# Optimization experiments

Measured on AMD Instinct MI355X. Metric: run time of the kernel, lower is better.

## Reference

```python
import jax, jax.numpy as jnp
import numpy as np

N = 20000        # nodes per type (ant, user)
E = 400000       # edges per relation
F_IN = 128       # args.user_num -> input feature dim
H = 10           # attention heads
D1, D2 = 16, 32  # per-head out channels of HGT layers 1 and 2
H1, H2 = H * D1, H * D2  # 160, 320


def _segment_softmax(logit, dst, n):
    m = jax.ops.segment_max(logit, dst, num_segments=n)
    e = jnp.exp(logit - m[dst])
    s = jax.ops.segment_sum(e, dst, num_segments=n)
    return e / (s[dst] + 1e-16)


def _hgt_layer(x_a, x_u, ei_au, ea_au, ei_ua, ea_ua,
               kw, kb, qw, qb, vw, vb, arel, mrel, prel, ew, eb, alw, alb, D):
    # per-node-type K/Q/V projections, reshaped to [N, H, D]
    def proj(x, w, b, i):
        return (x @ w[i] + b[i]).reshape(x.shape[0], H, D)
    k_a, q_a, v_a = proj(x_a, kw, kb, 0), proj(x_a, qw, qb, 0), proj(x_a, vw, vb, 0)
    k_u, q_u, v_u = proj(x_u, kw, kb, 1), proj(x_u, qw, qb, 1), proj(x_u, vw, vb, 1)
    scale = 1.0 / jnp.sqrt(jnp.float32(D))

    def relation(k_s, v_s, q_d, ei, ea, r, n_dst):
        # apply per-relation matrices at node granularity (cheaper than per-edge)
        kr = jnp.einsum('nhd,hde->nhe', k_s, arel[r])
        vr = jnp.einsum('nhd,hde->nhe', v_s, mrel[r])
        src, dst = ei[0], ei[1]
        # [E, H] attention logits: HGT dot-product * relation prior + edge-attr term
        logit = (q_d[dst] * kr[src]).sum(-1) * scale * prel[r] + ea @ ew[r] + eb[r]
        a = _segment_softmax(logit, dst, n_dst)
        msg = vr[src] * a[..., None]                        # [E, H, D]
        out = jax.ops.segment_sum(msg, dst, num_segments=n_dst)
        return out.reshape(n_dst, H * D)

    agg_u = relation(k_a, v_a, q_u, ei_au, ea_au, 0, x_u.shape[0])  # ant -> user
    agg_a = relation(k_u, v_u, q_a, ei_ua, ea_ua, 1, x_a.shape[0])  # user -> ant
    out_a = jax.nn.gelu(agg_a) @ alw[0] + alb[0]
    out_u = jax.nn.gelu(agg_u) @ alw[1] + alb[1]
    return out_a, out_u


def _bn(x, g, b):
    mu = x.mean(0)
    var = x.var(0)
    return (x - mu) / jnp.sqrt(var + 1e-5) * g + b


def _forward(x_ant, x_user, ea_au, ea_ua,
             l1_kw, l1_kb, l1_qw, l1_qb, l1_vw, l1_vb, l1_arel, l1_mrel, l1_prel, l1_ew, l1_eb, l1_alw, l1_alb,
             l2_kw, l2_kb, l2_qw, l2_qb, l2_vw, l2_vb, l2_arel, l2_mrel, l2_prel, l2_ew, l2_eb, l2_alw, l2_alb,
             lin1_w, lin1_b, bn_g, bn_b, lin2_wa, lin2_ba, lin2_wu, lin2_bu,
             ei_au, ei_ua):
    a, u = _hgt_layer(x_ant, x_user, ei_au, ea_au, ei_ua, ea_ua,
                      l1_kw, l1_kb, l1_qw, l1_qb, l1_vw, l1_vb,
                      l1_arel, l1_mrel, l1_prel, l1_ew, l1_eb, l1_alw, l1_alb, D1)
    a, u = jax.nn.elu(a), jax.nn.elu(u)
    a, u = _hgt_layer(a, u, ei_au, ea_au, ei_ua, ea_ua,
                      l2_kw, l2_kb, l2_qw, l2_qb, l2_vw, l2_vb,
                      l2_arel, l2_mrel, l2_prel, l2_ew, l2_eb, l2_alw, l2_alb, D2)
    a, u = jax.nn.elu(a), jax.nn.elu(u)
    a = jax.nn.elu(a @ lin1_w[0] + lin1_b[0])
    u = jax.nn.elu(u @ lin1_w[1] + lin1_b[1])
    a = _bn(a, bn_g[0], bn_b[0])
    u = _bn(u, bn_g[1], bn_b[1])
    a = a @ lin2_wa + lin2_ba       # [N, user_num]   beamforming weights
    u = u @ lin2_wu + lin2_bu       # [N, user_num+1] assignment logits
    # MM_Dict_ACT: power-normalize ant outputs, softmax user assignments
    a = a / jnp.sqrt((a * a).sum(-1, keepdims=True) + 1e-12)
    u = jax.nn.softmax(u, axis=-1)
    return a, u


def setup_inputs() -> dict:
    key = jax.random.key(0)
    ks = iter(jax.random.split(key, 64))
    nk = lambda: next(ks)
    rn = lambda shape, s=0.05: jax.random.normal(nk(), shape, dtype=jnp.float32) * s
    inp = {}
    inp['x_ant'] = rn((N, F_IN), 1.0)
    inp['x_user'] = rn((N, F_IN), 1.0)
    inp['ea_au'] = jax.random.uniform(nk(), (E, 1), dtype=jnp.float32)
    inp['ea_ua'] = jax.random.uniform(nk(), (E, 1), dtype=jnp.float32)

    def hgt_params(p, fin, d):
        hd = H * d
        inp[p + 'kw'] = rn((2, fin, hd)); inp[p + 'kb'] = jnp.zeros((2, hd))
        inp[p + 'qw'] = rn((2, fin, hd)); inp[p + 'qb'] = jnp.zeros((2, hd))
        inp[p + 'vw'] = rn((2, fin, hd)); inp[p + 'vb'] = jnp.zeros((2, hd))
        inp[p + 'arel'] = rn((2, H, d, d), 0.2)
        inp[p + 'mrel'] = rn((2, H, d, d), 0.2)
        inp[p + 'prel'] = jnp.ones((2, H), dtype=jnp.float32)
        inp[p + 'ew'] = rn((2, 1, H)); inp[p + 'eb'] = jnp.zeros((2, H))
        inp[p + 'alw'] = rn((2, hd, hd)); inp[p + 'alb'] = jnp.zeros((2, hd))

    hgt_params('l1_', F_IN, D1)
    hgt_params('l2_', H1, D2)
    inp['lin1_w'] = rn((2, H2, 512)); inp['lin1_b'] = jnp.zeros((2, 512))
    inp['bn_g'] = jnp.ones((2, 512), dtype=jnp.float32)
    inp['bn_b'] = jnp.zeros((2, 512), dtype=jnp.float32)
    inp['lin2_wa'] = rn((512, F_IN)); inp['lin2_ba'] = jnp.zeros((F_IN,))
    inp['lin2_wu'] = rn((512, F_IN + 1)); inp['lin2_bu'] = jnp.zeros((F_IN + 1,))
    inp['ei_au'] = jax.random.randint(nk(), (2, E), 0, N)
    inp['ei_ua'] = jax.random.randint(nk(), (2, E), 0, N)
    return inp


def reference(x_ant, x_user, ea_au, ea_ua,
              l1_kw, l1_kb, l1_qw, l1_qb, l1_vw, l1_vb, l1_arel, l1_mrel, l1_prel, l1_ew, l1_eb, l1_alw, l1_alb,
              l2_kw, l2_kb, l2_qw, l2_qb, l2_vw, l2_vb, l2_arel, l2_mrel, l2_prel, l2_ew, l2_eb, l2_alw, l2_alb,
              lin1_w, lin1_b, bn_g, bn_b, lin2_wa, lin2_ba, lin2_wu, lin2_bu,
              ei_au, ei_ua):
    return _forward(x_ant, x_user, ea_au, ea_ua,
                    l1_kw, l1_kb, l1_qw, l1_qb, l1_vw, l1_vb, l1_arel, l1_mrel, l1_prel, l1_ew, l1_eb, l1_alw, l1_alb,
                    l2_kw, l2_kb, l2_qw, l2_qb, l2_vw, l2_vb, l2_arel, l2_mrel, l2_prel, l2_ew, l2_eb, l2_alw, l2_alb,
                    lin1_w, lin1_b, bn_g, bn_b, lin2_wa, lin2_ba, lin2_wu, lin2_bu,
                    ei_au, ei_ua)
```

## Files before the change

kernel.cpp:

```cpp
#include <hip/hip_runtime.h>
#include <hip/hip_bf16.h>
#include <math.h>

#define N_NODES 20000
#define N_EDGES 400000
#define NH 10

typedef __attribute__((ext_vector_type(8))) short short8v;
typedef __attribute__((ext_vector_type(4))) float f32x4;

__device__ __forceinline__ float gelu_f(float x) {
    float x3 = x * x * x;
    return 0.5f * x * (1.0f + tanhf(0.7978845608028654f * (x + 0.044715f * x3)));
}
__device__ __forceinline__ float elu_f(float x) {
    return x > 0.0f ? x : (expf(x) - 1.0f);
}
__device__ __forceinline__ float bf_lo(unsigned int w) {
    return __uint_as_float(w << 16);
}
__device__ __forceinline__ float bf_hi(unsigned int w) {
    return __uint_as_float(w & 0xffff0000u);
}
__device__ __forceinline__ unsigned short f2b(float x) {
    unsigned int u = __float_as_uint(x);
    return (unsigned short)((u + 0x7fffu + ((u >> 16) & 1u)) >> 16);
}

struct GemmPair {
    const __hip_bfloat16 *A0, *A1, *W0, *W1;
    const float *b0, *b1;
    void *C0, *C1;
    int N0, N1;
};
template<int ACT, typename OUT>
__global__ __launch_bounds__(256) void gemm2_kernel(GemmPair P, int M, int K)
{
    constexpr int PITCH = 40;
    __shared__ __align__(16) unsigned short As[128 * PITCH];
    __shared__ __align__(16) unsigned short Bs[128 * PITCH];
    const int z = blockIdx.z;
    const __hip_bfloat16* A  = z ? P.A1 : P.A0;
    const __hip_bfloat16* WT = z ? P.W1 : P.W0;
    const float* bias = z ? P.b1 : P.b0;
    OUT* C = (OUT*)(z ? P.C1 : P.C0);
    const int N = z ? P.N1 : P.N0;

    const int tid = threadIdx.x;
    const int m0 = blockIdx.y * 128, n0 = blockIdx.x * 128;
    if (n0 >= N) return;
    const int w = tid >> 6, l = tid & 63;
    const int wr = w >> 1, wc = w & 1;
    const int lr = l & 15, lk = l >> 4;

    const int srow = tid >> 1, sseg = (tid & 1) * 16;
    const bool ainb = (m0 + srow) < M;
    const bool binb = (n0 + srow) < N;
    const __hip_bfloat16* aptr = A + (size_t)(m0 + srow) * K + sseg;
    const __hip_bfloat16* bptr = WT + (size_t)(n0 + srow) * K + sseg;

    int4 ra0, ra1, rb0, rb1;
    auto ld = [&](int k0) {
        ra0 = ainb ? *reinterpret_cast<const int4*>(aptr + k0)     : make_int4(0, 0, 0, 0);
        ra1 = ainb ? *reinterpret_cast<const int4*>(aptr + k0 + 8) : make_int4(0, 0, 0, 0);
        rb0 = binb ? *reinterpret_cast<const int4*>(bptr + k0)     : make_int4(0, 0, 0, 0);
        rb1 = binb ? *reinterpret_cast<const int4*>(bptr + k0 + 8) : make_int4(0, 0, 0, 0);
    };

    f32x4 acc[4][4] = {};
    ld(0);
    for (int k0 = 0; k0 < K; k0 += 32) {
        *reinterpret_cast<int4*>(&As[srow * PITCH + sseg])     = ra0;
        *reinterpret_cast<int4*>(&As[srow * PITCH + sseg + 8]) = ra1;
        *reinterpret_cast<int4*>(&Bs[srow * PITCH + sseg])     = rb0;
        *reinterpret_cast<int4*>(&Bs[srow * PITCH + sseg + 8]) = rb1;
        __syncthreads();
        if (k0 + 32 < K) ld(k0 + 32);
        short8v a[4], b[4];
        #pragma unroll
        for (int mi = 0; mi < 4; ++mi)
            a[mi] = *reinterpret_cast<const short8v*>(
                &As[(wr * 64 + mi * 16 + lr) * PITCH + lk * 8]);
        #pragma unroll
        for (int ni = 0; ni < 4; ++ni)
            b[ni] = *reinterpret_cast<const short8v*>(
                &Bs[(wc * 64 + ni * 16 + lr) * PITCH + lk * 8]);
        #pragma unroll
        for (int mi = 0; mi < 4; ++mi)
            #pragma unroll
            for (int ni = 0; ni < 4; ++ni)
                acc[mi][ni] = __builtin_amdgcn_mfma_f32_16x16x32_bf16(
                    a[mi], b[ni], acc[mi][ni], 0, 0, 0);
        __syncthreads();
    }
    #pragma unroll
    for (int ni = 0; ni < 4; ++ni) {
        const int col = n0 + wc * 64 + ni * 16 + lr;
        if (col >= N) continue;
        const float bv = bias[col];
        #pragma unroll
        for (int mi = 0; mi < 4; ++mi) {
            const int rb = m0 + wr * 64 + mi * 16 + lk * 4;
            #pragma unroll
            for (int j = 0; j < 4; ++j) {
                const int m = rb + j;
                if (m >= M) continue;
                float v = acc[mi][ni][j] + bv;
                if (ACT == 1) v = elu_f(v);
                if constexpr (sizeof(OUT) == 2)
                    C[(size_t)m * N + col] = __float2bfloat16(v);
                else
                    C[(size_t)m * N + col] = v;
            }
        }
    }
}

__global__ void transpose2_kernel(const float* in0, const float* in1,
                                  __hip_bfloat16* out0, __hip_bfloat16* out1,
                                  int K0, int N0, int K1, int N1)
{
    __shared__ float tile[32][33];
    const int z = blockIdx.z;
    const float* in = z ? in1 : in0;
    __hip_bfloat16* out = z ? out1 : out0;
    const int K = z ? K1 : K0, N = z ? N1 : N0;
    const int nb = blockIdx.x * 32, kb = blockIdx.y * 32;
    if (nb >= N || kb >= K) return;
    const int tx = threadIdx.x & 31, ty = threadIdx.x >> 5;
    for (int j = ty; j < 32; j += 8) {
        int k = kb + j, n = nb + tx;
        tile[j][tx] = (k < K && n < N) ? in[(size_t)k * N + n] : 0.f;
    }
    __syncthreads();
    for (int j = ty; j < 32; j += 8) {
        int n = nb + j, k = kb + tx;
        if (n < N && k < K) out[(size_t)n * K + k] = __float2bfloat16(tile[tx][j]);
    }
}

__global__ void convert_in_kernel(const float* __restrict__ in0, const float* __restrict__ in1,
                                  __hip_bfloat16* __restrict__ out0,
                                  __hip_bfloat16* __restrict__ out1, int n4)
{
    int i = blockIdx.x * blockDim.x + threadIdx.x;
    if (i >= n4) return;
    const float* in = blockIdx.y ? in1 : in0;
    __hip_bfloat16* out = blockIdx.y ? out1 : out0;
    float4 v = reinterpret_cast<const float4*>(in)[i];
    ushort4 b;
    b.x = f2b(v.x); b.y = f2b(v.y); b.z = f2b(v.z); b.w = f2b(v.w);
    reinterpret_cast<ushort4*>(out)[i] = b;
}

__global__ void prep_qkv2_kernel(const float* __restrict__ qw, const float* __restrict__ qb,
                                 const float* __restrict__ kw, const float* __restrict__ kb,
                                 const float* __restrict__ vw, const float* __restrict__ vb,
                                 const float* __restrict__ arel, const float* __restrict__ mrel,
                                 __hip_bfloat16* __restrict__ WT0, float* __restrict__ B0,
                                 __hip_bfloat16* __restrict__ WT1, float* __restrict__ B1,
                                 int fin, int D, int HD)
{
    const int type = blockIdx.y;
    const size_t woff = (size_t)type * fin * HD;
    const size_t roff = (size_t)type * NH * D * D;
    __hip_bfloat16* WT = type ? WT1 : WT0;
    float* BIAS = type ? B1 : B0;
    const int F1 = fin + 1;
    int tid = blockIdx.x * blockDim.x + threadIdx.x;
    if (tid >= 3 * HD * F1) return;
    const int f = tid % F1;
    const int col3 = tid / F1;
    const int sec = col3 / HD;
    const int col = col3 - sec * HD;
    float val;
    if (sec == 0) {
        val = (f < fin) ? qw[woff + (size_t)f * HD + col] : qb[type * HD + col];
    } else {
        const float* W = (sec == 1) ? kw : vw;
        const float* B = (sec == 1) ? kb : vb;
        const float* R = ((sec == 1) ? arel : mrel) + roff;
        const int h = col / D, e = col - h * D;
        const float* src = (f < fin) ? W + woff + (size_t)f * HD + h * D
                                     : B + type * HD + h * D;
        const float* r = R + (size_t)h * D * D + e;
        float acc = 0.f;
        for (int d = 0; d < D; ++d) acc = fmaf(src[d], r[(size_t)d * D], acc);
        val = acc;
    }
    if (f < fin) WT[(size_t)col3 * fin + f] = __float2bfloat16(val);
    else         BIAS[col3] = val;
}

template<int D>
__global__ __launch_bounds__(256) void edge_fused_kernel(
    const __hip_bfloat16* __restrict__ Ta, const __hip_bfloat16* __restrict__ Tu,
    const int* __restrict__ rp0, const int* __restrict__ src0, const float* __restrict__ eav0,
    const int* __restrict__ rp1, const int* __restrict__ src1, const float* __restrict__ eav1,
    const float* __restrict__ prel, const float* __restrict__ ew,
    const float* __restrict__ eb,
    __hip_bfloat16* __restrict__ outA, __hip_bfloat16* __restrict__ outU,
    float scale)
{
    constexpr int HD = NH * D;
    constexpr int S = 3 * HD;
    constexpr int C = 64;
    constexpr int POS = HD / 8;
    constexpr int G = (POS * 8 <= 256) ? 8 : 4;
    __shared__ float q_s[HD];
    __shared__ float ls[C][NH];
    __shared__ int   srcs[C];
    __shared__ float eas[C];
    __shared__ float prel_s[NH], ew_s[NH], eb_s[NH];

    const int b = blockIdx.x;
    const int rel = b & 1, dst = b >> 1;
    const int t = threadIdx.x;
    const __hip_bfloat16* Tkv = rel ? Tu : Ta;
    const __hip_bfloat16* Tq  = rel ? Ta : Tu;
    const int* rp    = rel ? rp1 : rp0;
    const int* srcA  = rel ? src1 : src0;
    const float* eav = rel ? eav1 : eav0;
    __hip_bfloat16* out = rel ? outA : outU;

    const int s0 = rp[dst], deg = rp[dst + 1] - s0;

    {
        const unsigned int* qrow = (const unsigned int*)(Tq + (size_t)dst * S);
        for (int i = t; i < HD / 2; i += 256) {
            unsigned int wd = qrow[i];
            q_s[2 * i]     = bf_lo(wd);
            q_s[2 * i + 1] = bf_hi(wd);
        }
    }
    if (t < NH) { prel_s[t] = prel[rel * NH + t]; ew_s[t] = ew[rel * NH + t];
                  eb_s[t] = eb[rel * NH + t]; }
    const int apos = t / G, ag = t % G;
    const int ah = (apos * 8) / D;
    float a8[8] = {};
    float ssum = 0.f;
    __syncthreads();

    for (int base = 0; base < deg; base += C) {
        const int cl = min(C, deg - base);
        if (t < cl) {
            srcs[t] = srcA[s0 + base + t];
            eas[t]  = eav[s0 + base + t];
        }
        __syncthreads();
        for (int item = t; item < cl * NH; item += 256) {
            const int p = item / NH, h = item - p * NH;
            const uint4* kr = (const uint4*)(Tkv + (size_t)srcs[p] * S + HD + h * D);
            const float* qh = q_s + h * D;
            float d0 = 0.f;
            #pragma unroll
            for (int c4 = 0; c4 < D / 8; ++c4) {
                const uint4 wd = kr[c4];
                const float* qq = qh + c4 * 8;
                d0 = fmaf(qq[0], bf_lo(wd.x), d0); d0 = fmaf(qq[1], bf_hi(wd.x), d0);
                d0 = fmaf(qq[2], bf_lo(wd.y), d0); d0 = fmaf(qq[3], bf_hi(wd.y), d0);
                d0 = fmaf(qq[4], bf_lo(wd.z), d0); d0 = fmaf(qq[5], bf_hi(wd.z), d0);
                d0 = fmaf(qq[6], bf_lo(wd.w), d0); d0 = fmaf(qq[7], bf_hi(wd.w), d0);
            }
            ls[p][h] = expf(d0 * scale * prel_s[h] + eas[p] * ew_s[h] + eb_s[h]);
        }
        __syncthreads();
        if (apos < POS) {
            for (int p = ag; p < cl; p += G) {
                const uint4* vr = (const uint4*)(Tkv + (size_t)srcs[p] * S + 2 * HD);
                const uint4 wd = vr[apos];
                const float wgt = ls[p][ah];
                ssum += wgt;
                a8[0] = fmaf(wgt, bf_lo(wd.x), a8[0]); a8[1] = fmaf(wgt, bf_hi(wd.x), a8[1]);
                a8[2] = fmaf(wgt, bf_lo(wd.y), a8[2]); a8[3] = fmaf(wgt, bf_hi(wd.y), a8[3]);
                a8[4] = fmaf(wgt, bf_lo(wd.z), a8[4]); a8[5] = fmaf(wgt, bf_hi(wd.z), a8[5]);
                a8[6] = fmaf(wgt, bf_lo(wd.w), a8[6]); a8[7] = fmaf(wgt, bf_hi(wd.w), a8[7]);
            }
        }
        __syncthreads();
    }
    if (apos < POS) {
        #pragma unroll
        for (int off = G / 2; off; off >>= 1) {
            #pragma unroll
            for (int j = 0; j < 8; ++j) a8[j] += __shfl_xor(a8[j], off);
            ssum += __shfl_xor(ssum, off);
        }
        if (ag == 0) {
            const float inv = 1.f / (ssum + 1e-16f);
            uint4 o;
            o.x = (unsigned int)f2b(gelu_f(a8[0] * inv)) |
                  ((unsigned int)f2b(gelu_f(a8[1] * inv)) << 16);
            o.y = (unsigned int)f2b(gelu_f(a8[2] * inv)) |
                  ((unsigned int)f2b(gelu_f(a8[3] * inv)) << 16);
            o.z = (unsigned int)f2b(gelu_f(a8[4] * inv)) |
                  ((unsigned int)f2b(gelu_f(a8[5] * inv)) << 16);
            o.w = (unsigned int)f2b(gelu_f(a8[6] * inv)) |
                  ((unsigned int)f2b(gelu_f(a8[7] * inv)) << 16);
            ((uint4*)(out + (size_t)dst * HD))[apos] = o;
        }
    }
}

__global__ void count2_kernel(const int* __restrict__ ei0, const int* __restrict__ ei1,
                              int* __restrict__ cnt0, int* __restrict__ cnt1)
{
    int e = blockIdx.x * blockDim.x + threadIdx.x;
    if (e >= N_EDGES) return;
    if (blockIdx.y == 0) atomicAdd(&cnt0[ei0[N_EDGES + e]], 1);
    else                 atomicAdd(&cnt1[ei1[N_EDGES + e]], 1);
}

__global__ void scatter2_kernel(const int* __restrict__ ei0, const float* __restrict__ ea0,
                                const int* __restrict__ ei1, const float* __restrict__ ea1,
                                int* __restrict__ cur0, int* __restrict__ cur1,
                                int* __restrict__ srcA0, float* __restrict__ eaA0,
                                int* __restrict__ srcA1, float* __restrict__ eaA1)
{
    int e = blockIdx.x * blockDim.x + threadIdx.x;
    if (e >= N_EDGES) return;
    const int y = blockIdx.y;
    const int* ei = y ? ei1 : ei0;
    const float* ea = y ? ea1 : ea0;
    int* cursor = y ? cur1 : cur0;
    int* srcA = y ? srcA1 : srcA0;
    float* eaA = y ? eaA1 : eaA0;
    int dst = ei[N_EDGES + e];
    int pos = atomicAdd(&cursor[dst], 1);
    srcA[pos] = ei[e];
    eaA[pos] = ea[e];
}

__global__ void exscan2_kernel(const int* __restrict__ cnt0, int* __restrict__ rp0, int* __restrict__ cur0,
                               const int* __restrict__ cnt1, int* __restrict__ rp1, int* __restrict__ cur1,
                               int n)
{
    __shared__ int buf[1024];
    __shared__ int carry;
    const int* cnt = blockIdx.x ? cnt1 : cnt0;
    int* rp = blockIdx.x ? rp1 : rp0;
    int* cursor = blockIdx.x ? cur1 : cur0;
    int t = threadIdx.x;
    if (t == 0) carry = 0;
    __syncthreads();
    for (int base = 0; base < n; base += 1024) {
        int v = (base + t < n) ? cnt[base + t] : 0;
        buf[t] = v;
        __syncthreads();
        for (int off = 1; off < 1024; off <<= 1) {
            int x = (t >= off) ? buf[t - off] : 0;
            __syncthreads();
            buf[t] += x;
            __syncthreads();
        }
        int excl = buf[t] - v + carry;
        if (base + t < n) { rp[base + t] = excl; cursor[base + t] = excl; }
        int total = buf[1023];
        __syncthreads();
        if (t == 0) carry += total;
        __syncthreads();
    }
    if (t == 0) rp[n] = carry;
}

__global__ void colstat2_kernel(const __hip_bfloat16* __restrict__ X0,
                                const __hip_bfloat16* __restrict__ X1,
                                float* __restrict__ sums, int M, int N)
{
    __shared__ float ls[256], lq[256];
    const int z = blockIdx.z;
    const __hip_bfloat16* X = z ? X1 : X0;
    float* sm = sums + z * 2 * N;
    int c = blockIdx.x * 64 + (threadIdx.x & 63);
    int rl = threadIdx.x >> 6;
    float s = 0.f, q = 0.f;
    for (int r = blockIdx.y * 4 + rl; r < M; r += gridDim.y * 4) {
        float v = __bfloat162float(X[(size_t)r * N + c]);
        s += v; q = fmaf(v, v, q);
    }
    ls[threadIdx.x] = s; lq[threadIdx.x] = q;
    __syncthreads();
    if (rl == 0) {
        s = ls[threadIdx.x] + ls[threadIdx.x + 64] + ls[threadIdx.x + 128] + ls[threadIdx.x + 192];
        q = lq[threadIdx.x] + lq[threadIdx.x + 64] + lq[threadIdx.x + 128] + lq[threadIdx.x + 192];
        atomicAdd(&sm[c], s);
        atomicAdd(&sm[N + c], q);
    }
}

__global__ void bn2_kernel(__hip_bfloat16* __restrict__ X0, __hip_bfloat16* __restrict__ X1,
                           const float* __restrict__ sums,
                           const float* __restrict__ g, const float* __restrict__ b,
                           int M, int N)
{
    int tid = blockIdx.x * blockDim.x + threadIdx.x;
    if (tid >= 2 * M * N) return;
    const int which = tid >= M * N;
    const int idx = tid - which * M * N;
    const int c = idx % N;
    __hip_bfloat16* X = which ? X1 : X0;
    const float* sm = sums + which * 2 * N;
    float mu = sm[c] / (float)M;
    float var = sm[N + c] / (float)M - mu * mu;
    float x = __bfloat162float(X[idx]);
    X[idx] = __float2bfloat16((x - mu) * rsqrtf(var + 1e-5f) * g[which * N + c]
                              + b[which * N + c]);
}

__global__ void epilogue_kernel(const float* __restrict__ XA, const float* __restrict__ XU,
                                float* __restrict__ out)
{
    const int row = blockIdx.x;
    const int l = threadIdx.x;
    if (blockIdx.y == 0) {
        const float* x = XA + (size_t)row * 128;
        float v0 = x[l], v1 = x[l + 64];
        float ss = v0 * v0 + v1 * v1;
        #pragma unroll
        for (int off = 32; off; off >>= 1) ss += __shfl_xor(ss, off);
        float inv = rsqrtf(ss + 1e-12f);
        out[(size_t)row * 128 + l] = v0 * inv;
        out[(size_t)row * 128 + l + 64] = v1 * inv;
    } else {
        const float* x = XU + (size_t)row * 129;
        float* o = out + (size_t)N_NODES * 128;
        float v0 = x[l], v1 = x[l + 64];
        float v2 = (l == 0) ? x[128] : -3.4e38f;
        float m = fmaxf(fmaxf(v0, v1), v2);
        #pragma unroll
        for (int off = 32; off; off >>= 1) m = fmaxf(m, __shfl_xor(m, off));
        float e0 = expf(v0 - m), e1 = expf(v1 - m);
        float e2 = (l == 0) ? expf(v2 - m) : 0.f;
        float s = e0 + e1 + e2;
        #pragma unroll
        for (int off = 32; off; off >>= 1) s += __shfl_xor(s, off);
        float inv = 1.f / s;
        o[(size_t)row * 129 + l] = e0 * inv;
        o[(size_t)row * 129 + l + 64] = e1 * inv;
        if (l == 0) o[(size_t)row * 129 + 128] = e2 * inv;
    }
}

template<int ACT, typename OUT>
static inline void launch_gemm2(const __hip_bfloat16* A0, const __hip_bfloat16* W0,
                                const float* b0, OUT* C0, int N0,
                                const __hip_bfloat16* A1, const __hip_bfloat16* W1,
                                const float* b1, OUT* C1, int N1,
                                int M, int K, hipStream_t s)
{
    GemmPair P = { A0, A1, W0, W1, b0, b1, (void*)C0, (void*)C1, N0, N1 };
    const int maxN = N0 > N1 ? N0 : N1;
    dim3 grid((maxN + 127) / 128, (M + 127) / 128, 2);
    gemm2_kernel<ACT, OUT><<<grid, 256, 0, s>>>(P, M, K);
}
static inline void launch_transpose2(const float* in0, const float* in1,
                                     __hip_bfloat16* out0, __hip_bfloat16* out1,
                                     int K0, int N0, int K1, int N1, hipStream_t s)
{
    const int maxN = N0 > N1 ? N0 : N1, maxK = K0 > K1 ? K0 : K1;
    dim3 grid((maxN + 31) / 32, (maxK + 31) / 32, 2);
    transpose2_kernel<<<grid, 256, 0, s>>>(in0, in1, out0, out1, K0, N0, K1, N1);
}

struct LayerParams {
    const float *kw, *kb, *qw, *qb, *vw, *vb, *arel, *mrel, *prel, *ew, *eb, *alw, *alb;
};

struct CsrRel { const int* rp; const int* src; const float* eav; };

template<int D>
static void run_layer(const LayerParams& P, int fin,
                      const __hip_bfloat16* xa, const __hip_bfloat16* xu,
                      __hip_bfloat16* TA, __hip_bfloat16* TU,
                      __hip_bfloat16* AGA, __hip_bfloat16* AGU,
                      __hip_bfloat16* ya, __hip_bfloat16* yu,
                      __hip_bfloat16* WT1, __hip_bfloat16* WT2,
                      float* BIAS1, float* BIAS2,
                      const CsrRel& au, const CsrRel& ua, hipStream_t s)
{
    const int HD = NH * D;
    const float scale = 1.0f / sqrtf((float)D);
    const int gP = (3 * HD * (fin + 1) + 255) / 256;

    {
        dim3 g(gP, 2);
        prep_qkv2_kernel<<<g, 256, 0, s>>>(P.qw, P.qb, P.kw, P.kb, P.vw, P.vb,
                                           P.arel, P.mrel, WT1, BIAS1, WT2, BIAS2,
                                           fin, D, HD);
    }
    launch_gemm2<0, __hip_bfloat16>(xa, WT1, BIAS1, TA, 3 * HD,
                                    xu, WT2, BIAS2, TU, 3 * HD, N_NODES, fin, s);

    edge_fused_kernel<D><<<2 * N_NODES, 256, 0, s>>>(
        TA, TU, au.rp, au.src, au.eav, ua.rp, ua.src, ua.eav,
        P.prel, P.ew, P.eb, AGA, AGU, scale);

    launch_transpose2(P.alw, P.alw + (size_t)HD * HD, WT1, WT2, HD, HD, HD, HD, s);
    launch_gemm2<1, __hip_bfloat16>(AGA, WT1, P.alb, ya, HD,
                                    AGU, WT2, P.alb + HD, yu, HD, N_NODES, HD, s);
}

extern "C" void kernel_launch(void* const* d_in, const int* in_sizes, int n_in,
                              void* d_out, int out_size, void* d_ws, size_t ws_size,
                              hipStream_t stream)
{
    const float* x_ant  = (const float*)d_in[0];
    const float* x_user = (const float*)d_in[1];
    const float* ea_au  = (const float*)d_in[2];
    const float* ea_ua  = (const float*)d_in[3];
    LayerParams L1 = {
        (const float*)d_in[4],  (const float*)d_in[5],  (const float*)d_in[6],
        (const float*)d_in[7],  (const float*)d_in[8],  (const float*)d_in[9],
        (const float*)d_in[10], (const float*)d_in[11], (const float*)d_in[12],
        (const float*)d_in[13], (const float*)d_in[14], (const float*)d_in[15],
        (const float*)d_in[16]
    };
    LayerParams L2 = {
        (const float*)d_in[17], (const float*)d_in[18], (const float*)d_in[19],
        (const float*)d_in[20], (const float*)d_in[21], (const float*)d_in[22],
        (const float*)d_in[23], (const float*)d_in[24], (const float*)d_in[25],
        (const float*)d_in[26], (const float*)d_in[27], (const float*)d_in[28],
        (const float*)d_in[29]
    };
    const float* lin1_w  = (const float*)d_in[30];
    const float* lin1_b  = (const float*)d_in[31];
    const float* bn_g    = (const float*)d_in[32];
    const float* bn_b    = (const float*)d_in[33];
    const float* lin2_wa = (const float*)d_in[34];
    const float* lin2_ba = (const float*)d_in[35];
    const float* lin2_wu = (const float*)d_in[36];
    const float* lin2_bu = (const float*)d_in[37];
    const int*   ei_au   = (const int*)d_in[38];
    const int*   ei_ua   = (const int*)d_in[39];

    char* P8 = (char*)d_ws;
    auto carve = [&](size_t bytes) { char* p = P8; P8 += (bytes + 255) & ~(size_t)255; return p; };
    __hip_bfloat16* XA  = (__hip_bfloat16*)carve((size_t)N_NODES * 128 * 2);
    __hip_bfloat16* XU  = (__hip_bfloat16*)carve((size_t)N_NODES * 128 * 2);
    __hip_bfloat16* TA  = (__hip_bfloat16*)carve((size_t)N_NODES * 960 * 2);
    __hip_bfloat16* TU  = (__hip_bfloat16*)carve((size_t)N_NODES * 960 * 2);
    __hip_bfloat16* AGA = (__hip_bfloat16*)carve((size_t)N_NODES * 320 * 2);
    __hip_bfloat16* AGU = (__hip_bfloat16*)carve((size_t)N_NODES * 320 * 2);
    __hip_bfloat16* YA  = (__hip_bfloat16*)carve((size_t)N_NODES * 320 * 2);
    __hip_bfloat16* YU  = (__hip_bfloat16*)carve((size_t)N_NODES * 320 * 2);
    __hip_bfloat16* L1A = (__hip_bfloat16*)carve((size_t)N_NODES * 512 * 2);
    __hip_bfloat16* L1U = (__hip_bfloat16*)carve((size_t)N_NODES * 512 * 2);
    __hip_bfloat16* WT1 = (__hip_bfloat16*)carve(960 * 320 * 2);
    __hip_bfloat16* WT2 = (__hip_bfloat16*)carve(960 * 320 * 2);
    float* BIAS1 = (float*)carve(960 * 4);
    float* BIAS2 = (float*)carve(960 * 4);
    float* STATS = (float*)carve(2048 * 4);
    int*   rp_au  = (int*)carve((N_NODES + 1) * 4);
    int*   rp_ua  = (int*)carve((N_NODES + 1) * 4);
    int*   src_au = (int*)carve((size_t)N_EDGES * 4);
    float* eav_au = (float*)carve((size_t)N_EDGES * 4);
    int*   src_ua = (int*)carve((size_t)N_EDGES * 4);
    float* eav_ua = (float*)carve((size_t)N_EDGES * 4);
    int*   cursor = (int*)carve((size_t)2 * N_NODES * 4);
    int*   counts = (int*)carve((size_t)2 * N_NODES * 4);

    const int gE = (N_EDGES + 255) / 256;

    hipMemsetAsync(counts, 0, 2 * N_NODES * sizeof(int), stream);
    {
        dim3 g(gE, 2);
        count2_kernel<<<g, 256, 0, stream>>>(ei_au, ei_ua, counts, counts + N_NODES);
    }
    exscan2_kernel<<<2, 1024, 0, stream>>>(counts, rp_au, cursor,
                                           counts + N_NODES, rp_ua, cursor + N_NODES,
                                           N_NODES);
    {
        dim3 g(gE, 2);
        scatter2_kernel<<<g, 256, 0, stream>>>(ei_au, ea_au, ei_ua, ea_ua,
                                               cursor, cursor + N_NODES,
                                               src_au, eav_au, src_ua, eav_ua);
    }
    CsrRel au = { rp_au, src_au, eav_au };
    CsrRel ua = { rp_ua, src_ua, eav_ua };

    {
        dim3 g((N_NODES * 128 / 4 + 255) / 256, 2);
        convert_in_kernel<<<g, 256, 0, stream>>>(x_ant, x_user, XA, XU, N_NODES * 128 / 4);
    }

    run_layer<16>(L1, 128, XA, XU, TA, TU, AGA, AGU, YA, YU,
                  WT1, WT2, BIAS1, BIAS2, au, ua, stream);

    run_layer<32>(L2, 160, YA, YU, TA, TU, AGA, AGU, TA, TU,
                  WT1, WT2, BIAS1, BIAS2, au, ua, stream);

    launch_transpose2(lin1_w, lin1_w + (size_t)320 * 512, WT1, WT2, 320, 512, 320, 512, stream);
    launch_gemm2<1, __hip_bfloat16>(TA, WT1, lin1_b, L1A, 512,
                                    TU, WT2, lin1_b + 512, L1U, 512, N_NODES, 320, stream);

    hipMemsetAsync(STATS, 0, 2048 * sizeof(float), stream);
    {
        dim3 g(8, 32, 2);
        colstat2_kernel<<<g, 256, 0, stream>>>(L1A, L1U, STATS, N_NODES, 512);
    }
    bn2_kernel<<<(2 * N_NODES * 512 + 255) / 256, 256, 0, stream>>>(
        L1A, L1U, STATS, bn_g, bn_b, N_NODES, 512);

    float* OUTA = (float*)AGA;
    float* OUTU = (float*)AGU;
    launch_transpose2(lin2_wa, lin2_wu, WT1, WT2, 512, 128, 512, 129, stream);
    launch_gemm2<0, float>(L1A, WT1, lin2_ba, OUTA, 128,
                           L1U, WT2, lin2_bu, OUTU, 129, N_NODES, 512, stream);
    {
        dim3 g(N_NODES, 2);
        epilogue_kernel<<<g, 64, 0, stream>>>(OUTA, OUTU, (float*)d_out);
    }
}
```

Before: 936.5 us.

## Batch all weight prep into two up-front launches and parallelize CSR scan

All per-layer weight transposes and the QKV/relation weight folding are hoisted into one prep launch and one 8-job transpose launch at the start, each writing its own dedicated buffer instead of reusing shared scratch. This removes four small serialized launches from the critical path between the large GEMM and edge kernels. Separately, the exclusive scan over 20000 counts now has each thread sum a contiguous chunk, does one block-wide scan, then writes the outputs, replacing about 20 sequential 1024-wide scan passes. Costs are extra buffer memory and a wasteful fixed grid sized for the largest job.

```diff
diff --git a/kernel.cpp b/kernel.cpp
--- a/kernel.cpp
+++ b/kernel.cpp
@@ -116,26 +116,24 @@
     }
 }
 
-__global__ void transpose2_kernel(const float* in0, const float* in1,
-                                  __hip_bfloat16* out0, __hip_bfloat16* out1,
-                                  int K0, int N0, int K1, int N1)
+struct TJob { const float* in; __hip_bfloat16* out; int K; int N; };
+struct TJobs8 { TJob j[8]; };
+__global__ void transpose8_kernel(TJobs8 J)
 {
     __shared__ float tile[32][33];
-    const int z = blockIdx.z;
-    const float* in = z ? in1 : in0;
-    __hip_bfloat16* out = z ? out1 : out0;
-    const int K = z ? K1 : K0, N = z ? N1 : N0;
+    const TJob job = J.j[blockIdx.z];
+    const int K = job.K, N = job.N;
     const int nb = blockIdx.x * 32, kb = blockIdx.y * 32;
     if (nb >= N || kb >= K) return;
     const int tx = threadIdx.x & 31, ty = threadIdx.x >> 5;
     for (int j = ty; j < 32; j += 8) {
         int k = kb + j, n = nb + tx;
-        tile[j][tx] = (k < K && n < N) ? in[(size_t)k * N + n] : 0.f;
+        tile[j][tx] = (k < K && n < N) ? job.in[(size_t)k * N + n] : 0.f;
     }
     __syncthreads();
     for (int j = ty; j < 32; j += 8) {
         int n = nb + j, k = kb + tx;
-        if (n < N && k < K) out[(size_t)n * K + k] = __float2bfloat16(tile[tx][j]);
+        if (n < N && k < K) job.out[(size_t)n * K + k] = __float2bfloat16(tile[tx][j]);
     }
 }
 
@@ -153,19 +151,32 @@
     reinterpret_cast<ushort4*>(out)[i] = b;
 }
 
-__global__ void prep_qkv2_kernel(const float* __restrict__ qw, const float* __restrict__ qb,
-                                 const float* __restrict__ kw, const float* __restrict__ kb,
-                                 const float* __restrict__ vw, const float* __restrict__ vb,
-                                 const float* __restrict__ arel, const float* __restrict__ mrel,
-                                 __hip_bfloat16* __restrict__ WT0, float* __restrict__ B0,
-                                 __hip_bfloat16* __restrict__ WT1, float* __restrict__ B1,
-                                 int fin, int D, int HD)
-{
-    const int type = blockIdx.y;
+struct PrepArgs {
+    const float *qw1, *qb1, *kw1, *kb1, *vw1, *vb1, *ar1, *mr1;
+    const float *qw2, *qb2, *kw2, *kb2, *vw2, *vb2, *ar2, *mr2;
+    __hip_bfloat16 *W1a, *W1u, *W2a, *W2u;
+    float *B1a, *B1u, *B2a, *B2u;
+};
+__global__ void prep_qkv4_kernel(PrepArgs A)
+{
+    const int y = blockIdx.y;
+    const int layer = y >> 1, type = y & 1;
+    const int D = layer ? 32 : 16;
+    const int fin = layer ? 160 : 128;
+    const int HD = NH * D;
+    const float* qw = layer ? A.qw2 : A.qw1;
+    const float* qb = layer ? A.qb2 : A.qb1;
+    const float* kw = layer ? A.kw2 : A.kw1;
+    const float* kb = layer ? A.kb2 : A.kb1;
+    const float* vw = layer ? A.vw2 : A.vw1;
+    const float* vb = layer ? A.vb2 : A.vb1;
+    const float* ar = layer ? A.ar2 : A.ar1;
+    const float* mr = layer ? A.mr2 : A.mr1;
+    __hip_bfloat16* WT = layer ? (type ? A.W2u : A.W2a) : (type ? A.W1u : A.W1a);
+    float* BIAS = layer ? (type ? A.B2u : A.B2a) : (type ? A.B1u : A.B1a);
     const size_t woff = (size_t)type * fin * HD;
     const size_t roff = (size_t)type * NH * D * D;
-    __hip_bfloat16* WT = type ? WT1 : WT0;
-    float* BIAS = type ? B1 : B0;
+
     const int F1 = fin + 1;
     int tid = blockIdx.x * blockDim.x + threadIdx.x;
     if (tid >= 3 * HD * F1) return;
@@ -179,7 +190,7 @@
     } else {
         const float* W = (sec == 1) ? kw : vw;
         const float* B = (sec == 1) ? kb : vb;
-        const float* R = ((sec == 1) ? arel : mrel) + roff;
+        const float* R = ((sec == 1) ? ar : mr) + roff;
         const int h = col / D, e = col - h * D;
         const float* src = (f < fin) ? W + woff + (size_t)f * HD + h * D
                                      : B + type * HD + h * D;
@@ -335,32 +346,35 @@
                                const int* __restrict__ cnt1, int* __restrict__ rp1, int* __restrict__ cur1,
                                int n)
 {
-    __shared__ int buf[1024];
-    __shared__ int carry;
+    __shared__ int sums[1024];
     const int* cnt = blockIdx.x ? cnt1 : cnt0;
     int* rp = blockIdx.x ? rp1 : rp0;
     int* cursor = blockIdx.x ? cur1 : cur0;
-    int t = threadIdx.x;
-    if (t == 0) carry = 0;
+    const int t = threadIdx.x;
+    const int CH = (n + 1023) / 1024;
+    const int b0 = t * CH;
+    int local = 0;
+    for (int i = 0; i < CH; ++i) {
+        int idx = b0 + i;
+        if (idx < n) local += cnt[idx];
+    }
+    sums[t] = local;
     __syncthreads();
-    for (int base = 0; base < n; base += 1024) {
-        int v = (base + t < n) ? cnt[base + t] : 0;
-        buf[t] = v;
+    for (int off = 1; off < 1024; off <<= 1) {
+        int x = (t >= off) ? sums[t - off] : 0;
         __syncthreads();
-        for (int off = 1; off < 1024; off <<= 1) {
-            int x = (t >= off) ? buf[t - off] : 0;
-            __syncthreads();
-            buf[t] += x;
-            __syncthreads();
-        }
-        int excl = buf[t] - v + carry;
-        if (base + t < n) { rp[base + t] = excl; cursor[base + t] = excl; }
-        int total = buf[1023];
+        sums[t] += x;
         __syncthreads();
-        if (t == 0) carry += total;
-        __syncthreads();
-    }
-    if (t == 0) rp[n] = carry;
+    }
+    int run = sums[t] - local;
+    for (int i = 0; i < CH; ++i) {
+        int idx = b0 + i;
+        if (idx < n) {
+            rp[idx] = run; cursor[idx] = run;
+            run += cnt[idx];
+        }
+    }
+    if (t == 1023) rp[n] = sums[1023];
 }
 
 __global__ void colstat2_kernel(const __hip_bfloat16* __restrict__ X0,
@@ -453,14 +467,6 @@
     dim3 grid((maxN + 127) / 128, (M + 127) / 128, 2);
     gemm2_kernel<ACT, OUT><<<grid, 256, 0, s>>>(P, M, K);
 }
-static inline void launch_transpose2(const float* in0, const float* in1,
-                                     __hip_bfloat16* out0, __hip_bfloat16* out1,
-                                     int K0, int N0, int K1, int N1, hipStream_t s)
-{
-    const int maxN = N0 > N1 ? N0 : N1, maxK = K0 > K1 ? K0 : K1;
-    dim3 grid((maxN + 31) / 32, (maxK + 31) / 32, 2);
-    transpose2_kernel<<<grid, 256, 0, s>>>(in0, in1, out0, out1, K0, N0, K1, N1);
-}
 
 struct LayerParams {
     const float *kw, *kb, *qw, *qb, *vw, *vb, *arel, *mrel, *prel, *ew, *eb, *alw, *alb;
@@ -474,30 +480,23 @@
                       __hip_bfloat16* TA, __hip_bfloat16* TU,
                       __hip_bfloat16* AGA, __hip_bfloat16* AGU,
                       __hip_bfloat16* ya, __hip_bfloat16* yu,
-                      __hip_bfloat16* WT1, __hip_bfloat16* WT2,
-                      float* BIAS1, float* BIAS2,
+                      const __hip_bfloat16* WQa, const __hip_bfloat16* WQu,
+                      const float* Ba, const float* Bu,
+                      const __hip_bfloat16* WALa, const __hip_bfloat16* WALu,
                       const CsrRel& au, const CsrRel& ua, hipStream_t s)
 {
     const int HD = NH * D;
     const float scale = 1.0f / sqrtf((float)D);
-    const int gP = (3 * HD * (fin + 1) + 255) / 256;
-
-    {
-        dim3 g(gP, 2);
-        prep_qkv2_kernel<<<g, 256, 0, s>>>(P.qw, P.qb, P.kw, P.kb, P.vw, P.vb,
-                                           P.arel, P.mrel, WT1, BIAS1, WT2, BIAS2,
-                                           fin, D, HD);
-    }
-    launch_gemm2<0, __hip_bfloat16>(xa, WT1, BIAS1, TA, 3 * HD,
-                                    xu, WT2, BIAS2, TU, 3 * HD, N_NODES, fin, s);
+
+    launch_gemm2<0, __hip_bfloat16>(xa, WQa, Ba, TA, 3 * HD,
+                                    xu, WQu, Bu, TU, 3 * HD, N_NODES, fin, s);
 
     edge_fused_kernel<D><<<2 * N_NODES, 256, 0, s>>>(
         TA, TU, au.rp, au.src, au.eav, ua.rp, ua.src, ua.eav,
         P.prel, P.ew, P.eb, AGA, AGU, scale);
 
-    launch_transpose2(P.alw, P.alw + (size_t)HD * HD, WT1, WT2, HD, HD, HD, HD, s);
-    launch_gemm2<1, __hip_bfloat16>(AGA, WT1, P.alb, ya, HD,
-                                    AGU, WT2, P.alb + HD, yu, HD, N_NODES, HD, s);
+    launch_gemm2<1, __hip_bfloat16>(AGA, WALa, P.alb, ya, HD,
+                                    AGU, WALu, P.alb + HD, yu, HD, N_NODES, HD, s);
 }
 
 extern "C" void kernel_launch(void* const* d_in, const int* in_sizes, int n_in,
@@ -545,10 +544,22 @@
     __hip_bfloat16* YU  = (__hip_bfloat16*)carve((size_t)N_NODES * 320 * 2);
     __hip_bfloat16* L1A = (__hip_bfloat16*)carve((size_t)N_NODES * 512 * 2);
     __hip_bfloat16* L1U = (__hip_bfloat16*)carve((size_t)N_NODES * 512 * 2);
-    __hip_bfloat16* WT1 = (__hip_bfloat16*)carve(960 * 320 * 2);
-    __hip_bfloat16* WT2 = (__hip_bfloat16*)carve(960 * 320 * 2);
-    float* BIAS1 = (float*)carve(960 * 4);
-    float* BIAS2 = (float*)carve(960 * 4);
+    __hip_bfloat16* WQ1A = (__hip_bfloat16*)carve(480 * 128 * 2);
+    __hip_bfloat16* WQ1U = (__hip_bfloat16*)carve(480 * 128 * 2);
+    __hip_bfloat16* WQ2A = (__hip_bfloat16*)carve(960 * 160 * 2);
+    __hip_bfloat16* WQ2U = (__hip_bfloat16*)carve(960 * 160 * 2);
+    __hip_bfloat16* WAL1A = (__hip_bfloat16*)carve(160 * 160 * 2);
+    __hip_bfloat16* WAL1U = (__hip_bfloat16*)carve(160 * 160 * 2);
+    __hip_bfloat16* WAL2A = (__hip_bfloat16*)carve(320 * 320 * 2);
+    __hip_bfloat16* WAL2U = (__hip_bfloat16*)carve(320 * 320 * 2);
+    __hip_bfloat16* WL1A = (__hip_bfloat16*)carve(512 * 320 * 2);
+    __hip_bfloat16* WL1U = (__hip_bfloat16*)carve(512 * 320 * 2);
+    __hip_bfloat16* WL2A = (__hip_bfloat16*)carve(128 * 512 * 2);
+    __hip_bfloat16* WL2U = (__hip_bfloat16*)carve(129 * 512 * 2);
+    float* B1A = (float*)carve(480 * 4);
+    float* B1U = (float*)carve(480 * 4);
+    float* B2A = (float*)carve(960 * 4);
+    float* B2U = (float*)carve(960 * 4);
     float* STATS = (float*)carve(2048 * 4);
     int*   rp_au  = (int*)carve((N_NODES + 1) * 4);
     int*   rp_ua  = (int*)carve((N_NODES + 1) * 4);
@@ -561,6 +572,30 @@
 
     const int gE = (N_EDGES + 255) / 256;
 
+    {
+        PrepArgs PA = {
+            L1.qw, L1.qb, L1.kw, L1.kb, L1.vw, L1.vb, L1.arel, L1.mrel,
+            L2.qw, L2.qb, L2.kw, L2.kb, L2.vw, L2.vb, L2.arel, L2.mrel,
+            WQ1A, WQ1U, WQ2A, WQ2U, B1A, B1U, B2A, B2U
+        };
+        dim3 g((3 * 320 * 161 + 255) / 256, 4);
+        prep_qkv4_kernel<<<g, 256, 0, stream>>>(PA);
+    }
+    {
+        TJobs8 J = {{
+            { L1.alw,                      WAL1A, 160, 160 },
+            { L1.alw + (size_t)160 * 160,  WAL1U, 160, 160 },
+            { L2.alw,                      WAL2A, 320, 320 },
+            { L2.alw + (size_t)320 * 320,  WAL2U, 320, 320 },
+            { lin1_w,                      WL1A,  320, 512 },
+            { lin1_w + (size_t)320 * 512,  WL1U,  320, 512 },
+            { lin2_wa,                     WL2A,  512, 128 },
+            { lin2_wu,                     WL2U,  512, 129 }
+        }};
+        dim3 g(512 / 32, 512 / 32, 8);
+        transpose8_kernel<<<g, 256, 0, stream>>>(J);
+    }
+
     hipMemsetAsync(counts, 0, 2 * N_NODES * sizeof(int), stream);
     {
         dim3 g(gE, 2);
@@ -584,14 +619,13 @@
     }
 
     run_layer<16>(L1, 128, XA, XU, TA, TU, AGA, AGU, YA, YU,
-                  WT1, WT2, BIAS1, BIAS2, au, ua, stream);
+                  WQ1A, WQ1U, B1A, B1U, WAL1A, WAL1U, au, ua, stream);
 
     run_layer<32>(L2, 160, YA, YU, TA, TU, AGA, AGU, TA, TU,
-                  WT1, WT2, BIAS1, BIAS2, au, ua, stream);
-
-    launch_transpose2(lin1_w, lin1_w + (size_t)320 * 512, WT1, WT2, 320, 512, 320, 512, stream);
-    launch_gemm2<1, __hip_bfloat16>(TA, WT1, lin1_b, L1A, 512,
-                                    TU, WT2, lin1_b + 512, L1U, 512, N_NODES, 320, stream);
+                  WQ2A, WQ2U, B2A, B2U, WAL2A, WAL2U, au, ua, stream);
+
+    launch_gemm2<1, __hip_bfloat16>(TA, WL1A, lin1_b, L1A, 512,
+                                    TU, WL1U, lin1_b + 512, L1U, 512, N_NODES, 320, stream);
 
     hipMemsetAsync(STATS, 0, 2048 * sizeof(float), stream);
     {
@@ -603,9 +637,8 @@
 
     float* OUTA = (float*)AGA;
     float* OUTU = (float*)AGU;
-    launch_transpose2(lin2_wa, lin2_wu, WT1, WT2, 512, 128, 512, 129, stream);
-    launch_gemm2<0, float>(L1A, WT1, lin2_ba, OUTA, 128,
-                           L1U, WT2, lin2_bu, OUTU, 129, N_NODES, 512, stream);
+    launch_gemm2<0, float>(L1A, WL2A, lin2_ba, OUTA, 128,
+                           L1U, WL2U, lin2_bu, OUTU, 129, N_NODES, 512, stream);
     {
         dim3 g(N_NODES, 2);
         epilogue_kernel<<<g, 64, 0, stream>>>(OUTA, OUTU, (float*)d_out);
```

After: 913.4 us. -2.5%, faster.
